# Kernel tuning notes

Hardware: AMD Instinct MI355X
Metric: run time of the kernel (lower is better)

The kernel has to match this reference:

```python
import jax, jax.numpy as jnp
from jax import lax
import numpy as np


def setup_inputs() -> dict:
    key = jax.random.key(0)
    x = jax.random.normal(key, (16, 1, 1536, 1536), dtype=jnp.float32)
    weight = jnp.ones((1, 1, 3, 3), dtype=jnp.float32) / 9.0
    return {"x": x, "weight": weight}


def _box3x3(z, weight):
    # z: (N, 1, H, W); zero padding=1 (torch conv2d default pad mode)
    return lax.conv_general_dilated(
        z, weight, window_strides=(1, 1), padding=((1, 1), (1, 1)),
        dimension_numbers=("NCHW", "OIHW", "NCHW"))


def _eig2x2(Axx, Axy, Ayy):
    # closed-form eigendecomposition of [[Axx, Axy], [Axy, Ayy]]
    T = Axx + Ayy
    D = Axx * Ayy - Axy * Axy
    s = jnp.sqrt(jnp.abs(T * T * 0.25 - D))
    l1 = T * 0.5 + s
    l2 = T * 0.5 - s
    e11 = l1 - Ayy
    e12 = Axy
    e21 = l2 - Ayy
    e22 = Axy
    small = jnp.abs(Axy) < 1e-9
    e11 = jnp.where(small, 1.0, e11)
    e12 = jnpp_zero = jnp.where(small, 0.0, e12)
    e21 = jnp.where(small, 0.0, e21)
    e22 = jnp.where(small, 1.0, e22)
    # sort so that the eigenvalue with smaller magnitude comes first
    lt = jnp.abs(l1) < jnp.abs(l2)
    lambda1 = jnp.where(lt, l1, l2)
    lambda2 = jnp.where(lt, l2, l1)
    e11_ = jnp.where(lt, e11, e21)
    e12_ = jnp.where(lt, e12, e22)
    e21_ = jnp.where(lt, e21, e11)
    e22_ = jnp.where(lt, e22, e12)
    # NOTE: original torch code has a typo (`labmda2_`), so only lambda1 gets ReLU
    lambda1 = jax.nn.relu(lambda1)
    return lambda1, lambda2, e11_, e12_, e21_, e22_


def reference(x, weight):
    n, c, h, w = x.shape
    # gx[..., 0] = x[..., 1] - x[..., 0]; gx[..., j] = x[..., j-1] - x[..., j]
    gx = jnp.concatenate([x[:, :, :, 1:2], x[:, :, :, :-1]], axis=3) - x
    gy = jnp.concatenate([x[:, :, 1:2, :], x[:, :, :-1, :]], axis=2) - x
    # per-channel box filter then mean over channels (c == 1 here)
    def smooth(z):
        zf = z.reshape(n * c, 1, h, w)
        out = _box3x3(zf, weight).reshape(n, c, h, w)
        return jnp.mean(out, axis=1)  # (N, H, W)
    Axx = smooth(gx * gx)
    Axy = smooth(gx * gy)
    Ayy = smooth(gy * gy)
    return _eig2x2(Axx, Axy, Ayy)
```

## Files before the change

### kernel.cpp

```cpp
#include <hip/hip_runtime.h>


typedef float f32x4 __attribute__((ext_vector_type(4)));
typedef float f32x2 __attribute__((ext_vector_type(2)));

constexpr int N = 16, H = 1536, W = 1536;
constexpr int TH = 16, TW = 128;
constexpr int XR = TH + 3;
constexpr int XQ = 34;
constexpr int XC = XQ * 4;
constexpr int CN = 130;
constexpr int CC = 132;

__global__ __launch_bounds__(256, 4)
void lsa_kernel(const float* __restrict__ x, float* __restrict__ out) {
    __shared__ float Xs[XR][XC];
    __shared__ float Cxx[TH][CC], Cxy[TH][CC], Cyy[TH][CC];

    const int tj0 = blockIdx.x * TW;
    const int ti0 = blockIdx.y * TH;
    const int n   = blockIdx.z;
    const float* __restrict__ xn = x + (size_t)n * (H * W);
    const int tid = threadIdx.x;
    const int rsub = tid >> 5;
    const int csub = tid & 31;

    for (int rr = rsub; rr < XR; rr += 8) {
        const int p = ti0 - 2 + rr;
        const float* rowp = xn + (size_t)p * W;
        const bool prow = (p >= 0) & (p < H);
        for (int cq = csub; cq < XQ; cq += 32) {
            const int qb = tj0 - 4 + 4 * cq;
            f32x4 v;
            if (prow && qb >= 0 && qb + 3 < W) {
                v = *reinterpret_cast<const f32x4*>(rowp + qb);
            } else {
                v.x = (prow && qb + 0 >= 0 && qb + 0 < W) ? rowp[qb + 0] : 0.f;
                v.y = (prow && qb + 1 >= 0 && qb + 1 < W) ? rowp[qb + 1] : 0.f;
                v.z = (prow && qb + 2 >= 0 && qb + 2 < W) ? rowp[qb + 2] : 0.f;
                v.w = (prow && qb + 3 >= 0 && qb + 3 < W) ? rowp[qb + 3] : 0.f;
            }
            *reinterpret_cast<f32x4*>(&Xs[rr][4 * cq]) = v;
        }
    }
    __syncthreads();

    for (int rr = rsub; rr < TH; rr += 8) {
        const int P0 = ti0 + rr;
        for (int ci = csub; ci < CN; ci += 32) {
            const int q = tj0 + ci - 1;
            float sxx = 0.f, sxy = 0.f, syy = 0.f;
            if (q >= 0 && q < W) {
                const int cc = ci + 3;
#pragma unroll
                for (int d = -1; d <= 1; ++d) {
                    const int p = P0 + d;
                    if (p >= 0 && p < H) {
                        const int RR = rr + d + 2;
                        const float xc = Xs[RR][cc];
                        const float xl = (q == 0) ? Xs[RR][cc + 1] : Xs[RR][cc - 1];
                        const float xu = (p == 0) ? Xs[RR + 1][cc] : Xs[RR - 1][cc];
                        const float gx = xl - xc;
                        const float gy = xu - xc;
                        sxx += gx * gx; sxy += gx * gy; syy += gy * gy;
                    }
                }
            }
            Cxx[rr][ci] = sxx; Cxy[rr][ci] = sxy; Cyy[rr][ci] = syy;
        }
    }
    __syncthreads();

    const size_t HW = (size_t)H * W;
    const size_t PLANE = (size_t)N * HW;
    const int cj = 4 * csub;
    const float inv9 = 1.0f / 9.0f;
    for (int rr = rsub; rr < TH; rr += 8) {
        const f32x4 a_xx = *reinterpret_cast<const f32x4*>(&Cxx[rr][cj]);
        const f32x2 b_xx = *reinterpret_cast<const f32x2*>(&Cxx[rr][cj + 4]);
        const f32x4 a_xy = *reinterpret_cast<const f32x4*>(&Cxy[rr][cj]);
        const f32x2 b_xy = *reinterpret_cast<const f32x2*>(&Cxy[rr][cj + 4]);
        const f32x4 a_yy = *reinterpret_cast<const f32x4*>(&Cyy[rr][cj]);
        const f32x2 b_yy = *reinterpret_cast<const f32x2*>(&Cyy[rr][cj + 4]);
        const float vxx[6] = {a_xx.x, a_xx.y, a_xx.z, a_xx.w, b_xx.x, b_xx.y};
        const float vxy[6] = {a_xy.x, a_xy.y, a_xy.z, a_xy.w, b_xy.x, b_xy.y};
        const float vyy[6] = {a_yy.x, a_yy.y, a_yy.z, a_yy.w, b_yy.x, b_yy.y};

        f32x4 o_l1, o_l2, o_e11, o_e12, o_e21, o_e22;
#pragma unroll
        for (int k = 0; k < 4; ++k) {
            const float Axx = (vxx[k] + vxx[k + 1] + vxx[k + 2]) * inv9;
            const float Axy = (vxy[k] + vxy[k + 1] + vxy[k + 2]) * inv9;
            const float Ayy = (vyy[k] + vyy[k + 1] + vyy[k + 2]) * inv9;

            const float T  = Axx + Ayy;
            const float Dd = Axx * Ayy - Axy * Axy;
            const float s  = sqrtf(fabsf(T * T * 0.25f - Dd));
            const float l1 = T * 0.5f + s;
            const float l2 = T * 0.5f - s;

            float e11 = l1 - Ayy, e12 = Axy;
            float e21 = l2 - Ayy, e22 = Axy;
            const bool small = fabsf(Axy) < 1e-9f;
            e11 = small ? 1.0f : e11;
            e12 = small ? 0.0f : e12;
            e21 = small ? 0.0f : e21;
            e22 = small ? 1.0f : e22;

            const bool lt = fabsf(l1) < fabsf(l2);
            o_l1[k]  = fmaxf(lt ? l1 : l2, 0.0f);
            o_l2[k]  = lt ? l2 : l1;
            o_e11[k] = lt ? e11 : e21;
            o_e12[k] = lt ? e12 : e22;
            o_e21[k] = lt ? e21 : e11;
            o_e22[k] = lt ? e22 : e12;
        }

        const size_t o = (size_t)n * HW + (size_t)(ti0 + rr) * W + (size_t)(tj0 + cj);
        __builtin_nontemporal_store(o_l1,  reinterpret_cast<f32x4*>(out + o));
        __builtin_nontemporal_store(o_l2,  reinterpret_cast<f32x4*>(out + PLANE + o));
        __builtin_nontemporal_store(o_e11, reinterpret_cast<f32x4*>(out + 2 * PLANE + o));
        __builtin_nontemporal_store(o_e12, reinterpret_cast<f32x4*>(out + 3 * PLANE + o));
        __builtin_nontemporal_store(o_e21, reinterpret_cast<f32x4*>(out + 4 * PLANE + o));
        __builtin_nontemporal_store(o_e22, reinterpret_cast<f32x4*>(out + 5 * PLANE + o));
    }
}

extern "C" void kernel_launch(void* const* d_in, const int* in_sizes, int n_in,
                              void* d_out, int out_size, void* d_ws, size_t ws_size,
                              hipStream_t stream) {
    const float* x = (const float*)d_in[0];
    float* out = (float*)d_out;

    dim3 grid(W / TW, H / TH, N);
    dim3 block(256);
    lsa_kernel<<<grid, block, 0, stream>>>(x, out);
}
```

Before: 208.5 us.

## Fuse vertical gradient sums into registers and drop intermediate shared tiles

Removes the Cxx/Cxy/Cyy shared-memory stage and its second barrier. Each thread now computes its six column sums straight from the input tile held in registers, then runs the eigen solve. Interior tiles take a branch-free path with vectorized LDS reads, while border tiles keep the guarded path. Launch bounds rise to 5 blocks per SM because LDS use drops. The cost is that neighbouring threads recompute overlapping column sums, and register pressure goes up.

```diff
diff --git a/kernel.cpp b/kernel.cpp
--- a/kernel.cpp
+++ b/kernel.cpp
@@ -4,26 +4,58 @@
 typedef float f32x4 __attribute__((ext_vector_type(4)));
 typedef float f32x2 __attribute__((ext_vector_type(2)));
 
-constexpr int N = 16, H = 1536, W = 1536;
+constexpr int N_ = 16, H = 1536, W = 1536;
 constexpr int TH = 16, TW = 128;
 constexpr int XR = TH + 3;
 constexpr int XQ = 34;
 constexpr int XC = XQ * 4;
-constexpr int CN = 130;
-constexpr int CC = 132;
 
-__global__ __launch_bounds__(256, 4)
+__device__ __forceinline__ void eig_emit(
+    const float Sxx[6], const float Sxy[6], const float Syy[6],
+    f32x4& o_l1, f32x4& o_l2, f32x4& o_e11, f32x4& o_e12, f32x4& o_e21, f32x4& o_e22) {
+    const float inv9 = 1.0f / 9.0f;
+#pragma unroll
+    for (int k = 0; k < 4; ++k) {
+        const float Axx = (Sxx[k] + Sxx[k + 1] + Sxx[k + 2]) * inv9;
+        const float Axy = (Sxy[k] + Sxy[k + 1] + Sxy[k + 2]) * inv9;
+        const float Ayy = (Syy[k] + Syy[k + 1] + Syy[k + 2]) * inv9;
+
+        const float T  = Axx + Ayy;
+        const float Dd = Axx * Ayy - Axy * Axy;
+        const float s  = sqrtf(fabsf(T * T * 0.25f - Dd));
+        const float l1 = T * 0.5f + s;
+        const float l2 = T * 0.5f - s;
+
+        float e11 = l1 - Ayy, e12 = Axy;
+        float e21 = l2 - Ayy, e22 = Axy;
+        const bool small = fabsf(Axy) < 1e-9f;
+        e11 = small ? 1.0f : e11;
+        e12 = small ? 0.0f : e12;
+        e21 = small ? 0.0f : e21;
+        e22 = small ? 1.0f : e22;
+
+        const bool lt = fabsf(l1) < fabsf(l2);
+        o_l1[k]  = fmaxf(lt ? l1 : l2, 0.0f);
+        o_l2[k]  = lt ? l2 : l1;
+        o_e11[k] = lt ? e11 : e21;
+        o_e12[k] = lt ? e12 : e22;
+        o_e21[k] = lt ? e21 : e11;
+        o_e22[k] = lt ? e22 : e12;
+    }
+}
+
+__global__ __launch_bounds__(256, 5)
 void lsa_kernel(const float* __restrict__ x, float* __restrict__ out) {
     __shared__ float Xs[XR][XC];
-    __shared__ float Cxx[TH][CC], Cxy[TH][CC], Cyy[TH][CC];
 
     const int tj0 = blockIdx.x * TW;
     const int ti0 = blockIdx.y * TH;
     const int n   = blockIdx.z;
     const float* __restrict__ xn = x + (size_t)n * (H * W);
-    const int tid = threadIdx.x;
+    const int tid  = threadIdx.x;
     const int rsub = tid >> 5;
     const int csub = tid & 31;
+    const int cj   = 4 * csub;
 
     for (int rr = rsub; rr < XR; rr += 8) {
         const int p = ti0 - 2 + rr;
@@ -45,84 +77,91 @@
     }
     __syncthreads();
 
-    for (int rr = rsub; rr < TH; rr += 8) {
-        const int P0 = ti0 + rr;
-        for (int ci = csub; ci < CN; ci += 32) {
-            const int q = tj0 + ci - 1;
-            float sxx = 0.f, sxy = 0.f, syy = 0.f;
-            if (q >= 0 && q < W) {
-                const int cc = ci + 3;
+    const size_t HW = (size_t)H * W;
+    const size_t PLANE = (size_t)N_ * HW;
+    float* const ob = out + (size_t)n * HW + (size_t)tj0 + cj;
+
+    const bool interior = (ti0 >= 2) & (ti0 <= H - TH - 1) & (tj0 >= 2) & (tj0 <= W - TW - 2);
+
+    if (interior) {
 #pragma unroll
-                for (int d = -1; d <= 1; ++d) {
-                    const int p = P0 + d;
-                    if (p >= 0 && p < H) {
-                        const int RR = rr + d + 2;
-                        const float xc = Xs[RR][cc];
-                        const float xl = (q == 0) ? Xs[RR][cc + 1] : Xs[RR][cc - 1];
-                        const float xu = (p == 0) ? Xs[RR + 1][cc] : Xs[RR - 1][cc];
-                        const float gx = xl - xc;
-                        const float gy = xu - xc;
-                        sxx += gx * gx; sxy += gx * gy; syy += gy * gy;
+        for (int rv = 0; rv < 2; ++rv) {
+            const int rr = rsub + 8 * rv;
+            float xv[4][7];
+#pragma unroll
+            for (int dr = 0; dr < 4; ++dr) {
+                const f32x2 a = *reinterpret_cast<const f32x2*>(&Xs[rr + dr][cj + 2]);
+                const f32x4 b = *reinterpret_cast<const f32x4*>(&Xs[rr + dr][cj + 4]);
+                xv[dr][0] = a.x; xv[dr][1] = a.y;
+                xv[dr][2] = b.x; xv[dr][3] = b.y; xv[dr][4] = b.z; xv[dr][5] = b.w;
+                xv[dr][6] = Xs[rr + dr][cj + 8];
+            }
+            float Sxx[6], Sxy[6], Syy[6];
+#pragma unroll
+            for (int m = 0; m < 6; ++m) {
+                float sxx = 0.f, sxy = 0.f, syy = 0.f;
+#pragma unroll
+                for (int d = 0; d < 3; ++d) {
+                    const float xc = xv[d + 1][m + 1];
+                    const float xl = xv[d + 1][m];
+                    const float xu = xv[d][m + 1];
+                    const float gx = xl - xc;
+                    const float gy = xu - xc;
+                    sxx = fmaf(gx, gx, sxx);
+                    sxy = fmaf(gx, gy, sxy);
+                    syy = fmaf(gy, gy, syy);
+                }
+                Sxx[m] = sxx; Sxy[m] = sxy; Syy[m] = syy;
+            }
+            f32x4 o1, o2, o3, o4, o5, o6;
+            eig_emit(Sxx, Sxy, Syy, o1, o2, o3, o4, o5, o6);
+            float* op = ob + (size_t)(ti0 + rr) * W;
+            __builtin_nontemporal_store(o1, reinterpret_cast<f32x4*>(op));
+            __builtin_nontemporal_store(o2, reinterpret_cast<f32x4*>(op + PLANE));
+            __builtin_nontemporal_store(o3, reinterpret_cast<f32x4*>(op + 2 * PLANE));
+            __builtin_nontemporal_store(o4, reinterpret_cast<f32x4*>(op + 3 * PLANE));
+            __builtin_nontemporal_store(o5, reinterpret_cast<f32x4*>(op + 4 * PLANE));
+            __builtin_nontemporal_store(o6, reinterpret_cast<f32x4*>(op + 5 * PLANE));
+        }
+    } else {
+#pragma unroll
+        for (int rv = 0; rv < 2; ++rv) {
+            const int rr = rsub + 8 * rv;
+            float Sxx[6], Sxy[6], Syy[6];
+#pragma unroll
+            for (int m = 0; m < 6; ++m) {
+                const int q = tj0 + cj - 1 + m;
+                float sxx = 0.f, sxy = 0.f, syy = 0.f;
+                if (q >= 0 && q < W) {
+                    const int cc = cj + m + 3;
+#pragma unroll
+                    for (int d = 0; d < 3; ++d) {
+                        const int p = ti0 + rr - 1 + d;
+                        if (p >= 0 && p < H) {
+                            const int RR = rr + d + 1;
+                            const float xc = Xs[RR][cc];
+                            const float xl = (q == 0) ? Xs[RR][cc + 1] : Xs[RR][cc - 1];
+                            const float xu = (p == 0) ? Xs[RR + 1][cc] : Xs[RR - 1][cc];
+                            const float gx = xl - xc;
+                            const float gy = xu - xc;
+                            sxx = fmaf(gx, gx, sxx);
+                            sxy = fmaf(gx, gy, sxy);
+                            syy = fmaf(gy, gy, syy);
+                        }
                     }
                 }
+                Sxx[m] = sxx; Sxy[m] = sxy; Syy[m] = syy;
             }
-            Cxx[rr][ci] = sxx; Cxy[rr][ci] = sxy; Cyy[rr][ci] = syy;
+            f32x4 o1, o2, o3, o4, o5, o6;
+            eig_emit(Sxx, Sxy, Syy, o1, o2, o3, o4, o5, o6);
+            float* op = ob + (size_t)(ti0 + rr) * W;
+            __builtin_nontemporal_store(o1, reinterpret_cast<f32x4*>(op));
+            __builtin_nontemporal_store(o2, reinterpret_cast<f32x4*>(op + PLANE));
+            __builtin_nontemporal_store(o3, reinterpret_cast<f32x4*>(op + 2 * PLANE));
+            __builtin_nontemporal_store(o4, reinterpret_cast<f32x4*>(op + 3 * PLANE));
+            __builtin_nontemporal_store(o5, reinterpret_cast<f32x4*>(op + 4 * PLANE));
+            __builtin_nontemporal_store(o6, reinterpret_cast<f32x4*>(op + 5 * PLANE));
         }
-    }
-    __syncthreads();
-
-    const size_t HW = (size_t)H * W;
-    const size_t PLANE = (size_t)N * HW;
-    const int cj = 4 * csub;
-    const float inv9 = 1.0f / 9.0f;
-    for (int rr = rsub; rr < TH; rr += 8) {
-        const f32x4 a_xx = *reinterpret_cast<const f32x4*>(&Cxx[rr][cj]);
-        const f32x2 b_xx = *reinterpret_cast<const f32x2*>(&Cxx[rr][cj + 4]);
-        const f32x4 a_xy = *reinterpret_cast<const f32x4*>(&Cxy[rr][cj]);
-        const f32x2 b_xy = *reinterpret_cast<const f32x2*>(&Cxy[rr][cj + 4]);
-        const f32x4 a_yy = *reinterpret_cast<const f32x4*>(&Cyy[rr][cj]);
-        const f32x2 b_yy = *reinterpret_cast<const f32x2*>(&Cyy[rr][cj + 4]);
-        const float vxx[6] = {a_xx.x, a_xx.y, a_xx.z, a_xx.w, b_xx.x, b_xx.y};
-        const float vxy[6] = {a_xy.x, a_xy.y, a_xy.z, a_xy.w, b_xy.x, b_xy.y};
-        const float vyy[6] = {a_yy.x, a_yy.y, a_yy.z, a_yy.w, b_yy.x, b_yy.y};
-
-        f32x4 o_l1, o_l2, o_e11, o_e12, o_e21, o_e22;
-#pragma unroll
-        for (int k = 0; k < 4; ++k) {
-            const float Axx = (vxx[k] + vxx[k + 1] + vxx[k + 2]) * inv9;
-            const float Axy = (vxy[k] + vxy[k + 1] + vxy[k + 2]) * inv9;
-            const float Ayy = (vyy[k] + vyy[k + 1] + vyy[k + 2]) * inv9;
-
-            const float T  = Axx + Ayy;
-            const float Dd = Axx * Ayy - Axy * Axy;
-            const float s  = sqrtf(fabsf(T * T * 0.25f - Dd));
-            const float l1 = T * 0.5f + s;
-            const float l2 = T * 0.5f - s;
-
-            float e11 = l1 - Ayy, e12 = Axy;
-            float e21 = l2 - Ayy, e22 = Axy;
-            const bool small = fabsf(Axy) < 1e-9f;
-            e11 = small ? 1.0f : e11;
-            e12 = small ? 0.0f : e12;
-            e21 = small ? 0.0f : e21;
-            e22 = small ? 1.0f : e22;
-
-            const bool lt = fabsf(l1) < fabsf(l2);
-            o_l1[k]  = fmaxf(lt ? l1 : l2, 0.0f);
-            o_l2[k]  = lt ? l2 : l1;
-            o_e11[k] = lt ? e11 : e21;
-            o_e12[k] = lt ? e12 : e22;
-            o_e21[k] = lt ? e21 : e11;
-            o_e22[k] = lt ? e22 : e12;
-        }
-
-        const size_t o = (size_t)n * HW + (size_t)(ti0 + rr) * W + (size_t)(tj0 + cj);
-        __builtin_nontemporal_store(o_l1,  reinterpret_cast<f32x4*>(out + o));
-        __builtin_nontemporal_store(o_l2,  reinterpret_cast<f32x4*>(out + PLANE + o));
-        __builtin_nontemporal_store(o_e11, reinterpret_cast<f32x4*>(out + 2 * PLANE + o));
-        __builtin_nontemporal_store(o_e12, reinterpret_cast<f32x4*>(out + 3 * PLANE + o));
-        __builtin_nontemporal_store(o_e21, reinterpret_cast<f32x4*>(out + 4 * PLANE + o));
-        __builtin_nontemporal_store(o_e22, reinterpret_cast<f32x4*>(out + 5 * PLANE + o));
     }
 }
 
@@ -132,7 +171,7 @@
     const float* x = (const float*)d_in[0];
     float* out = (float*)d_out;
 
-    dim3 grid(W / TW, H / TH, N);
+    dim3 grid(W / TW, H / TH, N_);
     dim3 block(256);
     lsa_kernel<<<grid, block, 0, stream>>>(x, out);
 }
```

Result: faster. 181.9 us (-12.8%).
